# Performance work log

Hardware: AMD Instinct MI355X
Metric: run time of the kernel (lower is better)

The kernel has to match this reference:

```python
import jax, jax.numpy as jnp
import numpy as np

N = 100000   # nodes
E = 1600000  # edges (avg degree 16)
D = 128      # feature dim (layer_sizes = [128, 128, 128])


def setup_inputs() -> dict:
    key = jax.random.key(0)
    ks = jax.random.split(key, 8)
    s = 1.0 / np.sqrt(D)  # glorot-ish scale for linear weights
    return {
        "x": jax.random.normal(ks[0], (N, D), jnp.float32),
        "edge_index": jax.random.randint(ks[1], (2, E), 0, N, dtype=jnp.int32),
        "perturb_first": jax.random.normal(ks[2], (N, D), jnp.float32) * 0.01,
        "perturb_last": jax.random.normal(ks[3], (N, D), jnp.float32) * 0.01,
        "W1": jax.random.normal(ks[4], (D, D), jnp.float32) * s,
        "b1": jnp.zeros((D,), jnp.float32),
        "W2": jax.random.normal(ks[5], (D, D), jnp.float32) * s,
        "b2": jnp.zeros((D,), jnp.float32),
    }


def reference(x, edge_index, perturb_first, perturb_last, W1, b1, W2, b2):
    n = x.shape[0]
    # PyG GCNConv: add self-loops, symmetric deg^{-1/2} normalization.
    loop = jnp.arange(n, dtype=edge_index.dtype)
    src = jnp.concatenate([edge_index[0], loop])  # [E+N]
    dst = jnp.concatenate([edge_index[1], loop])  # [E+N]
    deg = jax.ops.segment_sum(jnp.ones(dst.shape[0], x.dtype), dst, num_segments=n)
    dinv = jnp.where(deg > 0, 1.0 / jnp.sqrt(deg), 0.0)
    norm = (dinv[src] * dinv[dst])[:, None]  # [E+N, 1]

    def gcn_conv(h, W, b):
        h = h @ W.T                                   # linear (bias-free), [N, D]
        msg = h[src] * norm                           # gather + scale, [E+N, D]
        out = jax.ops.segment_sum(msg, dst, num_segments=n)  # scatter-add
        return out + b

    # forward only runs model[0] and model[3] (the two GCNConv layers);
    # norms and PReLU are skipped by the original forward.
    h = gcn_conv(x, W1, b1) + perturb_first
    out = gcn_conv(h, W2, b2) + perturb_last
    return out
```

## Files before the change

kernel.cpp:

```cpp
#include <hip/hip_runtime.h>
#include <math.h>

#define D 128
#define WS_PAD 132

typedef short bf16x8 __attribute__((ext_vector_type(8)));
typedef float f32x4 __attribute__((ext_vector_type(4)));

__device__ __forceinline__ unsigned short f2bf(float f) {
  unsigned u = __float_as_uint(f);
  u += 0x7FFFu + ((u >> 16) & 1u);
  return (unsigned short)(u >> 16);
}

__device__ __forceinline__ float bf2f(unsigned short h) {
  return __uint_as_float(((unsigned)h) << 16);
}


__global__ __launch_bounds__(256) void count_deg_kernel(const int* __restrict__ dst, int E,
                                                        int* __restrict__ deg,
                                                        int* __restrict__ rank,
                                                        const float* __restrict__ W2,
                                                        unsigned short* __restrict__ W2bf,
                                                        const float* __restrict__ W1,
                                                        unsigned short* __restrict__ W1h,
                                                        unsigned short* __restrict__ W1l) {
  int nbe = (E + 1023) >> 10;
  int b = blockIdx.x;
  if (b >= nbe) {
    if (W2bf == nullptr) return;
    int which = b - nbe;
    if (which < 8) {
      int t = which * 256 + threadIdx.x;
      #pragma unroll
      for (int q = 0; q < 2; ++q) {
        int idx = t + q * 2048;
        float4 w = ((const float4*)W2)[idx];
        ushort4 o;
        o.x = f2bf(w.x); o.y = f2bf(w.y); o.z = f2bf(w.z); o.w = f2bf(w.w);
        ((ushort4*)W2bf)[idx] = o;
      }
    } else {
      int t = (which - 8) * 256 + threadIdx.x;
      #pragma unroll
      for (int q = 0; q < 2; ++q) {
        int idx = t + q * 2048;
        float4 w = ((const float4*)W1)[idx];
        ushort4 hi, lo;
        hi.x = f2bf(w.x); lo.x = f2bf(w.x - bf2f(hi.x));
        hi.y = f2bf(w.y); lo.y = f2bf(w.y - bf2f(hi.y));
        hi.z = f2bf(w.z); lo.z = f2bf(w.z - bf2f(hi.z));
        hi.w = f2bf(w.w); lo.w = f2bf(w.w - bf2f(hi.w));
        ((ushort4*)W1h)[idx] = hi;
        ((ushort4*)W1l)[idx] = lo;
      }
    }
    return;
  }
  int e0 = (b * 256 + threadIdx.x) * 4;
  if (rank != nullptr) {
    if (e0 + 4 <= E && ((E & 3) == 0)) {
      int4 d = *(const int4*)(dst + e0);
      int r0 = atomicAdd(&deg[d.x], 1);
      int r1 = atomicAdd(&deg[d.y], 1);
      int r2 = atomicAdd(&deg[d.z], 1);
      int r3 = atomicAdd(&deg[d.w], 1);
      *(int4*)(rank + e0) = make_int4(r0, r1, r2, r3);
    } else {
      for (int e = e0; e < E && e < e0 + 4; ++e) rank[e] = atomicAdd(&deg[dst[e]], 1);
    }
  } else {
    for (int e = e0; e < E && e < e0 + 4; ++e) atomicAdd(&deg[dst[e]], 1);
  }
}


__global__ __launch_bounds__(256) void scan_blocksum_kernel(const int* __restrict__ deg, int n,
                                                            int* __restrict__ blockSums) {
  __shared__ int sm[256];
  int t = threadIdx.x;
  int i = blockIdx.x * 256 + t;
  sm[t] = (i < n) ? deg[i] : 0;
  __syncthreads();
  for (int off = 128; off > 0; off >>= 1) {
    if (t < off) sm[t] += sm[t + off];
    __syncthreads();
  }
  if (t == 0) blockSums[blockIdx.x] = sm[0];
}

__global__ __launch_bounds__(512) void scan_top_kernel(int* __restrict__ blockSums, int nb) {
  __shared__ int sm[512];
  int t = threadIdx.x;
  int v = (t < nb) ? blockSums[t] : 0;
  sm[t] = v;
  __syncthreads();
  for (int off = 1; off < 512; off <<= 1) {
    int x = (t >= off) ? sm[t - off] : 0;
    __syncthreads();
    sm[t] += x;
    __syncthreads();
  }
  if (t < nb) blockSums[t] = sm[t] - v;
}

__global__ __launch_bounds__(256) void scan_write_kernel(const int* __restrict__ deg, int n,
                                                         const int* __restrict__ blockSums,
                                                         int* __restrict__ ptr,
                                                         float* __restrict__ dinv) {
  __shared__ int sm[256];
  int t = threadIdx.x;
  int i = blockIdx.x * 256 + t;
  int v = (i < n) ? deg[i] : 0;
  sm[t] = v;
  __syncthreads();
  for (int off = 1; off < 256; off <<= 1) {
    int x = (t >= off) ? sm[t - off] : 0;
    __syncthreads();
    sm[t] += x;
    __syncthreads();
  }
  if (i < n) {
    int ex = blockSums[blockIdx.x] + sm[t] - v;
    ptr[i] = ex;
    dinv[i] = 1.0f / sqrtf((float)(v + 1));
    if (i == n - 1) ptr[n] = ex + v;
  }
}


__device__ __forceinline__ void gemm_body(const float* __restrict__ X,
                                          const float* __restrict__ W,
                                          const float* __restrict__ dinv,
                                          unsigned short* __restrict__ H, int n,
                                          int bid, int nblocks,
                                          float* __restrict__ Ws, float* __restrict__ Xs) {
  const int tid = threadIdx.x;
  const int tx = tid & 31;
  const int ty = tid >> 5;
  const int ntiles = (n + 31) >> 5;

  for (int tile = bid; tile < ntiles; tile += nblocks) {
    const int row0 = tile << 5;
    const int rows_here = min(32, n - row0);
    __syncthreads();
    {
      const float4* Xg = (const float4*)(X + (size_t)row0 * D);
      int tmax = rows_here * 32;
      for (int t = tid; t < tmax; t += 256) ((float4*)Xs)[t] = Xg[t];
    }
    float acc[4][4] = {{0.f}};
    #pragma unroll
    for (int kt = 0; kt < 128; kt += 64) {
      __syncthreads();
      for (int t = tid; t < 2048; t += 256) {
        int j  = t >> 4;
        int k4 = (t & 15) << 2;
        float4 w = ((const float4*)W)[j * 32 + (kt >> 2) + (t & 15)];
        Ws[(k4 + 0) * WS_PAD + j] = w.x;
        Ws[(k4 + 1) * WS_PAD + j] = w.y;
        Ws[(k4 + 2) * WS_PAD + j] = w.z;
        Ws[(k4 + 3) * WS_PAD + j] = w.w;
      }
      __syncthreads();
      #pragma unroll 4
      for (int k = 0; k < 64; ++k) {
        float4 w = *(const float4*)&Ws[k * WS_PAD + (tx << 2)];
        #pragma unroll
        for (int r = 0; r < 4; ++r) {
          float xv = Xs[(ty + 8 * r) * 128 + (kt + k)];
          acc[r][0] += xv * w.x;
          acc[r][1] += xv * w.y;
          acc[r][2] += xv * w.z;
          acc[r][3] += xv * w.w;
        }
      }
    }
    #pragma unroll
    for (int r = 0; r < 4; ++r) {
      int row = row0 + ty + 8 * r;
      if (row < n) {
        float s = dinv[row];
        unsigned h0 = f2bf(s * acc[r][0]);
        unsigned h1 = f2bf(s * acc[r][1]);
        unsigned h2 = f2bf(s * acc[r][2]);
        unsigned h3 = f2bf(s * acc[r][3]);
        ((uint2*)(H + (size_t)row * D))[tx] = make_uint2(h0 | (h1 << 16), h2 | (h3 << 16));
      }
    }
  }
}


__global__ __launch_bounds__(256) void fused_fill_gemm_kernel(
    const int* __restrict__ src, const int* __restrict__ dst,
    int* __restrict__ ptr, int* __restrict__ csr, int E,
    const float* __restrict__ X, const float* __restrict__ W,
    const float* __restrict__ dinv, unsigned short* __restrict__ H, int n) {
  __shared__ float Ws[64 * WS_PAD];
  __shared__ float Xs[32 * 128];
  int sub = blockIdx.x & 7;
  if (sub < 2) {
    int fb = (blockIdx.x >> 3) * 2 + sub;
    int stride = 512 * 256;
    for (int e = fb * 256 + threadIdx.x; e < E; e += stride) {
      int d = dst[e];
      int pos = atomicAdd(&ptr[d], 1);
      csr[pos] = src[e];
    }
  } else {
    int gb = (blockIdx.x >> 3) * 6 + (sub - 2);
    gemm_body(X, W, dinv, H, n, gb, 1536, Ws, Xs);
  }
}

__global__ __launch_bounds__(256) void gemm128_kernel(const float* __restrict__ X,
                                                      const float* __restrict__ W,
                                                      const float* __restrict__ dinv,
                                                      unsigned short* __restrict__ H, int n) {
  __shared__ float Ws[64 * WS_PAD];
  __shared__ float Xs[32 * 128];
  gemm_body(X, W, dinv, H, n, blockIdx.x, gridDim.x, Ws, Xs);
}


#define FUSED_GRID 2048
#define G1_PITCH 136

__global__ __launch_bounds__(256) void fused_fill_mfma_kernel(
    const int* __restrict__ src, const int* __restrict__ dst,
    const int* __restrict__ ptr, const int* __restrict__ rank,
    int* __restrict__ csr, int E,
    const float* __restrict__ X,
    const unsigned short* __restrict__ W1h, const unsigned short* __restrict__ W1l,
    const float* __restrict__ dinv, unsigned short* __restrict__ H, int n) {
  __shared__ unsigned short Ths[32 * G1_PITCH];
  __shared__ unsigned short Tls[32 * G1_PITCH];
  int sub = blockIdx.x & 7;
  if (sub < 2) {
    int fb = (blockIdx.x >> 3) * 2 + sub;
    const int T8 = 512 * 256 * 8;
    int t = fb * 256 + threadIdx.x;
    const bool al16 = ((E & 3) == 0);
    for (int e0 = t * 8; e0 < E; e0 += T8) {
      if (e0 + 8 <= E && al16) {
        int4 d0 = ((const int4*)(dst + e0))[0];
        int4 d1 = ((const int4*)(dst + e0))[1];
        int4 s0 = ((const int4*)(src + e0))[0];
        int4 s1 = ((const int4*)(src + e0))[1];
        int4 r0 = ((const int4*)(rank + e0))[0];
        int4 r1 = ((const int4*)(rank + e0))[1];
        int p0 = ptr[d0.x] + r0.x;
        int p1 = ptr[d0.y] + r0.y;
        int p2 = ptr[d0.z] + r0.z;
        int p3 = ptr[d0.w] + r0.w;
        int p4 = ptr[d1.x] + r1.x;
        int p5 = ptr[d1.y] + r1.y;
        int p6 = ptr[d1.z] + r1.z;
        int p7 = ptr[d1.w] + r1.w;
        csr[p0] = s0.x; csr[p1] = s0.y; csr[p2] = s0.z; csr[p3] = s0.w;
        csr[p4] = s1.x; csr[p5] = s1.y; csr[p6] = s1.z; csr[p7] = s1.w;
      } else {
        for (int e = e0; e < E && e < e0 + 8; ++e)
          csr[ptr[dst[e]] + rank[e]] = src[e];
      }
    }
  } else {
    int gb = (blockIdx.x >> 3) * 6 + (sub - 2);
    const int tid = threadIdx.x;
    const int wv = tid >> 6;
    const int lane = tid & 63;
    const int m = lane & 15;
    const int quad = lane >> 4;
    const int mt = wv >> 1;
    const int ntb = (wv & 1) * 4;
    const int ntiles = (n + 31) >> 5;

    for (int tile = gb; tile < ntiles; tile += 1536) {
      const int row0 = tile << 5;
      const int rows_here = min(32, n - row0);
      __syncthreads();
      {
        const float4* Xg = (const float4*)(X + (size_t)row0 * D);
        int tmax = rows_here * 32;
        for (int t = tid; t < tmax; t += 256) {
          float4 xv = Xg[t];
          int r = t >> 5, c4 = (t & 31) << 2;
          ushort4 hi, lo;
          hi.x = f2bf(xv.x); lo.x = f2bf(xv.x - bf2f(hi.x));
          hi.y = f2bf(xv.y); lo.y = f2bf(xv.y - bf2f(hi.y));
          hi.z = f2bf(xv.z); lo.z = f2bf(xv.z - bf2f(hi.z));
          hi.w = f2bf(xv.w); lo.w = f2bf(xv.w - bf2f(hi.w));
          *(ushort4*)&Ths[r * G1_PITCH + c4] = hi;
          *(ushort4*)&Tls[r * G1_PITCH + c4] = lo;
        }
      }
      __syncthreads();

      f32x4 acc0 = {0.f, 0.f, 0.f, 0.f};
      f32x4 acc1 = {0.f, 0.f, 0.f, 0.f};
      f32x4 acc2 = {0.f, 0.f, 0.f, 0.f};
      f32x4 acc3 = {0.f, 0.f, 0.f, 0.f};
      #pragma unroll
      for (int s = 0; s < 4; ++s) {
        int k = (s << 5) + (quad << 3);
        bf16x8 ah = *(const bf16x8*)&Ths[(mt * 16 + m) * G1_PITCH + k];
        bf16x8 al = *(const bf16x8*)&Tls[(mt * 16 + m) * G1_PITCH + k];
        bf16x8 bh0 = *(const bf16x8*)&W1h[(size_t)((ntb + 0) * 16 + m) * 128 + k];
        bf16x8 bl0 = *(const bf16x8*)&W1l[(size_t)((ntb + 0) * 16 + m) * 128 + k];
        acc0 = __builtin_amdgcn_mfma_f32_16x16x32_bf16(ah, bh0, acc0, 0, 0, 0);
        acc0 = __builtin_amdgcn_mfma_f32_16x16x32_bf16(al, bh0, acc0, 0, 0, 0);
        acc0 = __builtin_amdgcn_mfma_f32_16x16x32_bf16(ah, bl0, acc0, 0, 0, 0);
        bf16x8 bh1 = *(const bf16x8*)&W1h[(size_t)((ntb + 1) * 16 + m) * 128 + k];
        bf16x8 bl1 = *(const bf16x8*)&W1l[(size_t)((ntb + 1) * 16 + m) * 128 + k];
        acc1 = __builtin_amdgcn_mfma_f32_16x16x32_bf16(ah, bh1, acc1, 0, 0, 0);
        acc1 = __builtin_amdgcn_mfma_f32_16x16x32_bf16(al, bh1, acc1, 0, 0, 0);
        acc1 = __builtin_amdgcn_mfma_f32_16x16x32_bf16(ah, bl1, acc1, 0, 0, 0);
        bf16x8 bh2 = *(const bf16x8*)&W1h[(size_t)((ntb + 2) * 16 + m) * 128 + k];
        bf16x8 bl2 = *(const bf16x8*)&W1l[(size_t)((ntb + 2) * 16 + m) * 128 + k];
        acc2 = __builtin_amdgcn_mfma_f32_16x16x32_bf16(ah, bh2, acc2, 0, 0, 0);
        acc2 = __builtin_amdgcn_mfma_f32_16x16x32_bf16(al, bh2, acc2, 0, 0, 0);
        acc2 = __builtin_amdgcn_mfma_f32_16x16x32_bf16(ah, bl2, acc2, 0, 0, 0);
        bf16x8 bh3 = *(const bf16x8*)&W1h[(size_t)((ntb + 3) * 16 + m) * 128 + k];
        bf16x8 bl3 = *(const bf16x8*)&W1l[(size_t)((ntb + 3) * 16 + m) * 128 + k];
        acc3 = __builtin_amdgcn_mfma_f32_16x16x32_bf16(ah, bh3, acc3, 0, 0, 0);
        acc3 = __builtin_amdgcn_mfma_f32_16x16x32_bf16(al, bh3, acc3, 0, 0, 0);
        acc3 = __builtin_amdgcn_mfma_f32_16x16x32_bf16(ah, bl3, acc3, 0, 0, 0);
      }
      #pragma unroll
      for (int r = 0; r < 4; ++r) {
        int row = mt * 16 + (quad << 2) + r;
        int g = row0 + row;
        if (g < n) {
          float sc = dinv[g];
          H[(size_t)g * D + (ntb + 0) * 16 + m] = f2bf(sc * acc0[r]);
          H[(size_t)g * D + (ntb + 1) * 16 + m] = f2bf(sc * acc1[r]);
          H[(size_t)g * D + (ntb + 2) * 16 + m] = f2bf(sc * acc2[r]);
          H[(size_t)g * D + (ntb + 3) * 16 + m] = f2bf(sc * acc3[r]);
        }
      }
    }
  }
}


__device__ __forceinline__ void gather_row(const int* __restrict__ csr, int start, int end,
                                           const unsigned* __restrict__ Hu,
                                           int i, int lane, float& ax, float& ay) {
  unsigned v = Hu[(size_t)i * 64 + lane];
  ax = __uint_as_float(v << 16);
  ay = __uint_as_float(v & 0xFFFF0000u);
  int e = start;
  for (; e + 8 <= end; e += 8) {
    unsigned w0 = Hu[(size_t)csr[e + 0] * 64 + lane];
    unsigned w1 = Hu[(size_t)csr[e + 1] * 64 + lane];
    unsigned w2 = Hu[(size_t)csr[e + 2] * 64 + lane];
    unsigned w3 = Hu[(size_t)csr[e + 3] * 64 + lane];
    unsigned w4 = Hu[(size_t)csr[e + 4] * 64 + lane];
    unsigned w5 = Hu[(size_t)csr[e + 5] * 64 + lane];
    unsigned w6 = Hu[(size_t)csr[e + 6] * 64 + lane];
    unsigned w7 = Hu[(size_t)csr[e + 7] * 64 + lane];
    ax += __uint_as_float(w0 << 16) + __uint_as_float(w1 << 16) +
          __uint_as_float(w2 << 16) + __uint_as_float(w3 << 16) +
          __uint_as_float(w4 << 16) + __uint_as_float(w5 << 16) +
          __uint_as_float(w6 << 16) + __uint_as_float(w7 << 16);
    ay += __uint_as_float(w0 & 0xFFFF0000u) + __uint_as_float(w1 & 0xFFFF0000u) +
          __uint_as_float(w2 & 0xFFFF0000u) + __uint_as_float(w3 & 0xFFFF0000u) +
          __uint_as_float(w4 & 0xFFFF0000u) + __uint_as_float(w5 & 0xFFFF0000u) +
          __uint_as_float(w6 & 0xFFFF0000u) + __uint_as_float(w7 & 0xFFFF0000u);
  }
  for (; e < end; ++e) {
    unsigned w = Hu[(size_t)csr[e] * 64 + lane];
    ax += __uint_as_float(w << 16);
    ay += __uint_as_float(w & 0xFFFF0000u);
  }
}


__global__ __launch_bounds__(256, 8) void gather_kernel(const int* __restrict__ csr,
                                                        const int* __restrict__ rptr,
                                                        const float* __restrict__ dinv,
                                                        const unsigned* __restrict__ Hu,
                                                        const float* __restrict__ bias,
                                                        const float* __restrict__ perturb,
                                                        float* __restrict__ out, int n) {
  int i = (blockIdx.x << 2) + (threadIdx.x >> 6);
  if (i >= n) return;
  int lane = threadIdx.x & 63;
  float ax, ay;
  gather_row(csr, rptr[i], rptr[i + 1], Hu, i, lane, ax, ay);
  float di = dinv[i];
  float2 p = ((const float2*)(perturb + (size_t)i * D))[lane];
  float2 o;
  o.x = bias[2 * lane + 0] + p.x + di * ax;
  o.y = bias[2 * lane + 1] + p.y + di * ay;
  ((float2*)(out + (size_t)i * D))[lane] = o;
}

__global__ __launch_bounds__(256, 8) void gather_kernel_old(const int* __restrict__ csr,
                                                            const int* __restrict__ rend,
                                                            const float* __restrict__ dinv,
                                                            const unsigned* __restrict__ Hu,
                                                            const float* __restrict__ bias,
                                                            const float* __restrict__ perturb,
                                                            float* __restrict__ out, int n) {
  int i = (blockIdx.x << 2) + (threadIdx.x >> 6);
  if (i >= n) return;
  int lane = threadIdx.x & 63;
  int start = (i == 0) ? 0 : rend[i - 1];
  float ax, ay;
  gather_row(csr, start, rend[i], Hu, i, lane, ax, ay);
  float di = dinv[i];
  float2 p = ((const float2*)(perturb + (size_t)i * D))[lane];
  float2 o;
  o.x = bias[2 * lane + 0] + p.x + di * ax;
  o.y = bias[2 * lane + 1] + p.y + di * ay;
  ((float2*)(out + (size_t)i * D))[lane] = o;
}


#define GG_PITCH 136

__global__ __launch_bounds__(512, 8) void gather_gemm_kernel(
    const int* __restrict__ csr, const int* __restrict__ rptr,
    const float* __restrict__ dinv, const unsigned* __restrict__ Hu,
    const float* __restrict__ bias, const float* __restrict__ perturb,
    const unsigned short* __restrict__ W2bf, unsigned short* __restrict__ H2, int n) {
  __shared__ unsigned short Ts[32 * GG_PITCH];
  const int tid = threadIdx.x;
  const int wv = tid >> 6;
  const int lane = tid & 63;
  const int base = blockIdx.x << 5;

  #pragma unroll
  for (int j = 0; j < 4; ++j) {
    int row = (wv << 2) + j;
    int i = base + row;
    if (i < n) {
      float ax, ay;
      gather_row(csr, rptr[i], rptr[i + 1], Hu, i, lane, ax, ay);
      float di = dinv[i];
      float2 p = ((const float2*)(perturb + (size_t)i * D))[lane];
      float ox = bias[2 * lane + 0] + p.x + di * ax;
      float oy = bias[2 * lane + 1] + p.y + di * ay;
      unsigned pack = (unsigned)f2bf(ox) | ((unsigned)f2bf(oy) << 16);
      *(unsigned*)&Ts[row * GG_PITCH + (lane << 1)] = pack;
    }
  }
  __syncthreads();

  const int mt = wv >> 2;
  const int nt0 = wv & 3;
  const int m = lane & 15;
  const int quad = lane >> 4;
  const unsigned short* Wrow0 = W2bf + (size_t)(nt0 * 16 + m) * 128;
  const unsigned short* Wrow1 = W2bf + (size_t)((nt0 + 4) * 16 + m) * 128;
  f32x4 acc0 = {0.f, 0.f, 0.f, 0.f};
  f32x4 acc1 = {0.f, 0.f, 0.f, 0.f};
  #pragma unroll
  for (int s = 0; s < 4; ++s) {
    int k = (s << 5) + (quad << 3);
    bf16x8 a  = *(const bf16x8*)&Ts[(mt * 16 + m) * GG_PITCH + k];
    bf16x8 b0 = *(const bf16x8*)&Wrow0[k];
    bf16x8 b1 = *(const bf16x8*)&Wrow1[k];
    acc0 = __builtin_amdgcn_mfma_f32_16x16x32_bf16(a, b0, acc0, 0, 0, 0);
    acc1 = __builtin_amdgcn_mfma_f32_16x16x32_bf16(a, b1, acc1, 0, 0, 0);
  }
  #pragma unroll
  for (int r = 0; r < 4; ++r) {
    int row = mt * 16 + (quad << 2) + r;
    int g = base + row;
    if (g < n) {
      float s = dinv[g];
      H2[(size_t)g * D + nt0 * 16 + m]       = f2bf(s * acc0[r]);
      H2[(size_t)g * D + (nt0 + 4) * 16 + m] = f2bf(s * acc1[r]);
    }
  }
}


extern "C" void kernel_launch(void* const* d_in, const int* in_sizes, int n_in,
                              void* d_out, int out_size, void* d_ws, size_t ws_size,
                              hipStream_t stream) {
  const float* x  = (const float*)d_in[0];
  const int*   ei = (const int*)d_in[1];
  const float* pf = (const float*)d_in[2];
  const float* pl = (const float*)d_in[3];
  const float* W1 = (const float*)d_in[4];
  const float* b1 = (const float*)d_in[5];
  const float* W2 = (const float*)d_in[6];
  const float* b2 = (const float*)d_in[7];
  float* out = (float*)d_out;

  const int n = in_sizes[0] / D;
  const int E = in_sizes[1] / 2;
  const int* src = ei;
  const int* dst = ei + E;

  int*   deg       = (int*)d_ws;
  float* dinv      = (float*)d_ws + n;
  int*   ptr       = (int*)d_ws + 2 * n;
  int*   blockSums = (int*)d_ws + 3 * n + 1;
  int*   csr       = (int*)d_ws + 3 * n + 1 + 512;
  size_t a1_off = ((size_t)(3 * n + 1 + 512 + E) * 4 + 255) & ~(size_t)255;
  unsigned short* A1 = (unsigned short*)((char*)d_ws + a1_off);
  unsigned short* A2 = A1 + (size_t)n * D;
  unsigned short* W2bf = A2 + (size_t)n * D;
  unsigned short* W1h  = W2bf + 128 * 128;
  unsigned short* W1l  = W1h + 128 * 128;
  int* rank = (int*)A2;
  size_t needed = a1_off + (2 * (size_t)n * D + 3 * 128 * 128) * sizeof(unsigned short);
  const bool fused_l2 = (ws_size >= needed);

  const int nb_n = (n + 255) / 256;
  const int nb_e4 = (E + 1023) / 1024;
  const int nb_g = (n + 3) / 4;

  hipMemsetAsync(deg, 0, (size_t)n * sizeof(int), stream);
  count_deg_kernel<<<nb_e4 + 16, 256, 0, stream>>>(
      dst, E, deg, fused_l2 ? rank : (int*)nullptr, W2,
      fused_l2 ? W2bf : (unsigned short*)nullptr, W1, W1h, W1l);
  scan_blocksum_kernel<<<nb_n, 256, 0, stream>>>(deg, n, blockSums);
  scan_top_kernel<<<1, 512, 0, stream>>>(blockSums, nb_n);
  scan_write_kernel<<<nb_n, 256, 0, stream>>>(deg, n, blockSums, ptr, dinv);

  if (fused_l2) {
    fused_fill_mfma_kernel<<<FUSED_GRID, 256, 0, stream>>>(src, dst, ptr, rank, csr, E, x,
                                                           W1h, W1l, dinv, A1, n);
    gather_gemm_kernel<<<(n + 31) / 32, 512, 0, stream>>>(csr, ptr, dinv, (const unsigned*)A1,
                                                          b1, pf, W2bf, A2, n);
    gather_kernel<<<nb_g, 256, 0, stream>>>(csr, ptr, dinv, (const unsigned*)A2, b2, pl, out, n);
  } else {
    fused_fill_gemm_kernel<<<FUSED_GRID, 256, 0, stream>>>(src, dst, ptr, csr, E, x, W1, dinv, A1, n);
    gather_kernel_old<<<nb_g, 256, 0, stream>>>(csr, ptr, dinv, (const unsigned*)A1, b1, pf, out, n);
    gemm128_kernel<<<1024, 256, 0, stream>>>(out, W2, dinv, A1, n);
    gather_kernel_old<<<nb_g, 256, 0, stream>>>(csr, ptr, dinv, (const unsigned*)A1, b2, pl, out, n);
  }
}
```

Before: 525.7 us.

## Gather four rows per wavefront with 16-byte loads per lane

Rewrites the SpMM gather so each wavefront handles four destination rows at once, with 16 lanes per row each loading a uint4 (eight bf16 values) per neighbor. Both the fused gather+GEMM kernel and the final gather kernel use the new quad layout, and the grids shrink to match. The aim is fewer, wider memory transactions and more independent rows in flight per wave. The cost is divergence across the four rows when their degrees differ, since the loop runs until the longest row is done.

```diff
diff --git a/kernel.cpp b/kernel.cpp
--- a/kernel.cpp
+++ b/kernel.cpp
@@ -16,6 +16,9 @@
 __device__ __forceinline__ float bf2f(unsigned short h) {
   return __uint_as_float(((unsigned)h) << 16);
 }
+
+__device__ __forceinline__ float bflo(unsigned u) { return __uint_as_float(u << 16); }
+__device__ __forceinline__ float bfhi(unsigned u) { return __uint_as_float(u & 0xFFFF0000u); }
 
 
 __global__ __launch_bounds__(256) void count_deg_kernel(const int* __restrict__ dst, int E,
@@ -345,32 +348,39 @@
 }
 
 
-__device__ __forceinline__ void gather_row(const int* __restrict__ csr, int start, int end,
-                                           const unsigned* __restrict__ Hu,
-                                           int i, int lane, float& ax, float& ay) {
+__device__ __forceinline__ void gather_quad(const int* __restrict__ csr, int start, int end,
+                                            const uint4* __restrict__ Hu4, int i, int sub,
+                                            float acc[8]) {
+  uint4 v = Hu4[(size_t)i * 16 + sub];
+  acc[0] = bflo(v.x); acc[1] = bfhi(v.x);
+  acc[2] = bflo(v.y); acc[3] = bfhi(v.y);
+  acc[4] = bflo(v.z); acc[5] = bfhi(v.z);
+  acc[6] = bflo(v.w); acc[7] = bfhi(v.w);
+  int e = start;
+  while (__ballot(e < end)) {
+    uint4 w0 = {0u, 0u, 0u, 0u}, w1 = {0u, 0u, 0u, 0u};
+    if (e < end)     w0 = Hu4[(size_t)csr[e] * 16 + sub];
+    if (e + 1 < end) w1 = Hu4[(size_t)csr[e + 1] * 16 + sub];
+    acc[0] += bflo(w0.x); acc[1] += bfhi(w0.x);
+    acc[2] += bflo(w0.y); acc[3] += bfhi(w0.y);
+    acc[4] += bflo(w0.z); acc[5] += bfhi(w0.z);
+    acc[6] += bflo(w0.w); acc[7] += bfhi(w0.w);
+    acc[0] += bflo(w1.x); acc[1] += bfhi(w1.x);
+    acc[2] += bflo(w1.y); acc[3] += bfhi(w1.y);
+    acc[4] += bflo(w1.z); acc[5] += bfhi(w1.z);
+    acc[6] += bflo(w1.w); acc[7] += bfhi(w1.w);
+    e += 2;
+  }
+}
+
+
+__device__ __forceinline__ void gather_row_legacy(const int* __restrict__ csr, int start, int end,
+                                                  const unsigned* __restrict__ Hu,
+                                                  int i, int lane, float& ax, float& ay) {
   unsigned v = Hu[(size_t)i * 64 + lane];
   ax = __uint_as_float(v << 16);
   ay = __uint_as_float(v & 0xFFFF0000u);
-  int e = start;
-  for (; e + 8 <= end; e += 8) {
-    unsigned w0 = Hu[(size_t)csr[e + 0] * 64 + lane];
-    unsigned w1 = Hu[(size_t)csr[e + 1] * 64 + lane];
-    unsigned w2 = Hu[(size_t)csr[e + 2] * 64 + lane];
-    unsigned w3 = Hu[(size_t)csr[e + 3] * 64 + lane];
-    unsigned w4 = Hu[(size_t)csr[e + 4] * 64 + lane];
-    unsigned w5 = Hu[(size_t)csr[e + 5] * 64 + lane];
-    unsigned w6 = Hu[(size_t)csr[e + 6] * 64 + lane];
-    unsigned w7 = Hu[(size_t)csr[e + 7] * 64 + lane];
-    ax += __uint_as_float(w0 << 16) + __uint_as_float(w1 << 16) +
-          __uint_as_float(w2 << 16) + __uint_as_float(w3 << 16) +
-          __uint_as_float(w4 << 16) + __uint_as_float(w5 << 16) +
-          __uint_as_float(w6 << 16) + __uint_as_float(w7 << 16);
-    ay += __uint_as_float(w0 & 0xFFFF0000u) + __uint_as_float(w1 & 0xFFFF0000u) +
-          __uint_as_float(w2 & 0xFFFF0000u) + __uint_as_float(w3 & 0xFFFF0000u) +
-          __uint_as_float(w4 & 0xFFFF0000u) + __uint_as_float(w5 & 0xFFFF0000u) +
-          __uint_as_float(w6 & 0xFFFF0000u) + __uint_as_float(w7 & 0xFFFF0000u);
-  }
-  for (; e < end; ++e) {
+  for (int e = start; e < end; ++e) {
     unsigned w = Hu[(size_t)csr[e] * 64 + lane];
     ax += __uint_as_float(w << 16);
     ay += __uint_as_float(w & 0xFFFF0000u);
@@ -385,17 +395,34 @@
                                                         const float* __restrict__ bias,
                                                         const float* __restrict__ perturb,
                                                         float* __restrict__ out, int n) {
-  int i = (blockIdx.x << 2) + (threadIdx.x >> 6);
-  if (i >= n) return;
-  int lane = threadIdx.x & 63;
-  float ax, ay;
-  gather_row(csr, rptr[i], rptr[i + 1], Hu, i, lane, ax, ay);
-  float di = dinv[i];
-  float2 p = ((const float2*)(perturb + (size_t)i * D))[lane];
-  float2 o;
-  o.x = bias[2 * lane + 0] + p.x + di * ax;
-  o.y = bias[2 * lane + 1] + p.y + di * ay;
-  ((float2*)(out + (size_t)i * D))[lane] = o;
+  const int lane = threadIdx.x & 63;
+  const int g = lane >> 4;
+  const int sub = lane & 15;
+  int i = (blockIdx.x << 4) + ((threadIdx.x >> 6) << 2) + g;
+  bool valid = i < n;
+  int ic = valid ? i : (n - 1);
+  int start = rptr[ic];
+  int end = valid ? rptr[ic + 1] : start;
+  float acc[8];
+  gather_quad(csr, start, end, (const uint4*)Hu, ic, sub, acc);
+  if (valid) {
+    float di = dinv[i];
+    float4 b0 = *(const float4*)&bias[sub * 8];
+    float4 b1 = *(const float4*)&bias[sub * 8 + 4];
+    float4 p0 = *(const float4*)&perturb[(size_t)i * D + sub * 8];
+    float4 p1 = *(const float4*)&perturb[(size_t)i * D + sub * 8 + 4];
+    float4 o0, o1;
+    o0.x = b0.x + p0.x + di * acc[0];
+    o0.y = b0.y + p0.y + di * acc[1];
+    o0.z = b0.z + p0.z + di * acc[2];
+    o0.w = b0.w + p0.w + di * acc[3];
+    o1.x = b1.x + p1.x + di * acc[4];
+    o1.y = b1.y + p1.y + di * acc[5];
+    o1.z = b1.z + p1.z + di * acc[6];
+    o1.w = b1.w + p1.w + di * acc[7];
+    *(float4*)&out[(size_t)i * D + sub * 8] = o0;
+    *(float4*)&out[(size_t)i * D + sub * 8 + 4] = o1;
+  }
 }
 
 __global__ __launch_bounds__(256, 8) void gather_kernel_old(const int* __restrict__ csr,
@@ -410,7 +437,7 @@
   int lane = threadIdx.x & 63;
   int start = (i == 0) ? 0 : rend[i - 1];
   float ax, ay;
-  gather_row(csr, start, rend[i], Hu, i, lane, ax, ay);
+  gather_row_legacy(csr, start, rend[i], Hu, i, lane, ax, ay);
   float di = dinv[i];
   float2 p = ((const float2*)(perturb + (size_t)i * D))[lane];
   float2 o;
@@ -433,19 +460,33 @@
   const int lane = tid & 63;
   const int base = blockIdx.x << 5;
 
-  #pragma unroll
-  for (int j = 0; j < 4; ++j) {
-    int row = (wv << 2) + j;
-    int i = base + row;
-    if (i < n) {
-      float ax, ay;
-      gather_row(csr, rptr[i], rptr[i + 1], Hu, i, lane, ax, ay);
+  {
+    const int g = lane >> 4;
+    const int sub = lane & 15;
+    int row_in_block = (wv << 2) + g;
+    int i = base + row_in_block;
+    bool valid = i < n;
+    int ic = valid ? i : (n - 1);
+    int start = rptr[ic];
+    int end = valid ? rptr[ic + 1] : start;
+    float acc[8];
+    gather_quad(csr, start, end, (const uint4*)Hu, ic, sub, acc);
+    if (valid) {
       float di = dinv[i];
-      float2 p = ((const float2*)(perturb + (size_t)i * D))[lane];
-      float ox = bias[2 * lane + 0] + p.x + di * ax;
-      float oy = bias[2 * lane + 1] + p.y + di * ay;
-      unsigned pack = (unsigned)f2bf(ox) | ((unsigned)f2bf(oy) << 16);
-      *(unsigned*)&Ts[row * GG_PITCH + (lane << 1)] = pack;
+      float4 b0 = *(const float4*)&bias[sub * 8];
+      float4 b1 = *(const float4*)&bias[sub * 8 + 4];
+      float4 p0 = *(const float4*)&perturb[(size_t)i * D + sub * 8];
+      float4 p1 = *(const float4*)&perturb[(size_t)i * D + sub * 8 + 4];
+      unsigned q0 = (unsigned)f2bf(b0.x + p0.x + di * acc[0]) |
+                    ((unsigned)f2bf(b0.y + p0.y + di * acc[1]) << 16);
+      unsigned q1 = (unsigned)f2bf(b0.z + p0.z + di * acc[2]) |
+                    ((unsigned)f2bf(b0.w + p0.w + di * acc[3]) << 16);
+      unsigned q2 = (unsigned)f2bf(b1.x + p1.x + di * acc[4]) |
+                    ((unsigned)f2bf(b1.y + p1.y + di * acc[5]) << 16);
+      unsigned q3 = (unsigned)f2bf(b1.z + p1.z + di * acc[6]) |
+                    ((unsigned)f2bf(b1.w + p1.w + di * acc[7]) << 16);
+      uint4 pack = make_uint4(q0, q1, q2, q3);
+      *(uint4*)&Ts[row_in_block * GG_PITCH + sub * 8] = pack;
     }
   }
   __syncthreads();
@@ -470,11 +511,11 @@
   #pragma unroll
   for (int r = 0; r < 4; ++r) {
     int row = mt * 16 + (quad << 2) + r;
-    int g = base + row;
-    if (g < n) {
-      float s = dinv[g];
-      H2[(size_t)g * D + nt0 * 16 + m]       = f2bf(s * acc0[r]);
-      H2[(size_t)g * D + (nt0 + 4) * 16 + m] = f2bf(s * acc1[r]);
+    int gg = base + row;
+    if (gg < n) {
+      float s = dinv[gg];
+      H2[(size_t)gg * D + nt0 * 16 + m]       = f2bf(s * acc0[r]);
+      H2[(size_t)gg * D + (nt0 + 4) * 16 + m] = f2bf(s * acc1[r]);
     }
   }
 }
@@ -515,7 +556,8 @@
 
   const int nb_n = (n + 255) / 256;
   const int nb_e4 = (E + 1023) / 1024;
-  const int nb_g = (n + 3) / 4;
+  const int nb_g16 = (n + 15) / 16;
+  const int nb_g4 = (n + 3) / 4;
 
   hipMemsetAsync(deg, 0, (size_t)n * sizeof(int), stream);
   count_deg_kernel<<<nb_e4 + 16, 256, 0, stream>>>(
@@ -530,11 +572,11 @@
                                                            W1h, W1l, dinv, A1, n);
     gather_gemm_kernel<<<(n + 31) / 32, 512, 0, stream>>>(csr, ptr, dinv, (const unsigned*)A1,
                                                           b1, pf, W2bf, A2, n);
-    gather_kernel<<<nb_g, 256, 0, stream>>>(csr, ptr, dinv, (const unsigned*)A2, b2, pl, out, n);
+    gather_kernel<<<nb_g16, 256, 0, stream>>>(csr, ptr, dinv, (const unsigned*)A2, b2, pl, out, n);
   } else {
     fused_fill_gemm_kernel<<<FUSED_GRID, 256, 0, stream>>>(src, dst, ptr, csr, E, x, W1, dinv, A1, n);
-    gather_kernel_old<<<nb_g, 256, 0, stream>>>(csr, ptr, dinv, (const unsigned*)A1, b1, pf, out, n);
+    gather_kernel_old<<<nb_g4, 256, 0, stream>>>(csr, ptr, dinv, (const unsigned*)A1, b1, pf, out, n);
     gemm128_kernel<<<1024, 256, 0, stream>>>(out, W2, dinv, A1, n);
-    gather_kernel_old<<<nb_g, 256, 0, stream>>>(csr, ptr, dinv, (const unsigned*)A1, b2, pl, out, n);
-  }
-}
+    gather_kernel_old<<<nb_g4, 256, 0, stream>>>(csr, ptr, dinv, (const unsigned*)A1, b2, pl, out, n);
+  }
+}
```

After: 490.5 us. 6.7% less time.
